# Kernel optimization log

Measured on AMD Instinct MI355X. Metric: run time of the kernel, lower is better.

The kernel has to match this reference:

```python
import jax, jax.numpy as jnp
import numpy as np
import math

B, N, D, H = 32, 512, 512, 8  # batch, num_neurons(=seq len=input_size), d_model, n_head
DH = D // H


def setup_inputs() -> dict:
    key = jax.random.key(0)
    ks = jax.random.split(key, 20)
    g = lambda k, shape, fan_in: jax.random.normal(k, shape, dtype=jnp.float32) / np.sqrt(fan_in)
    return {
        "x": jax.random.normal(ks[0], (B, N), dtype=jnp.float32),
        # per-neuron Linear(1, d_model): weight [N, D], bias [N, D]
        "W_emb": g(ks[1], (N, D), 1),
        "b_emb": g(ks[2], (N, D), 1),
        # MHA projections (stored [in, out])
        "Wq": g(ks[3], (D, D), D), "bq": jnp.zeros((D,), jnp.float32),
        "Wk": g(ks[4], (D, D), D), "bk": jnp.zeros((D,), jnp.float32),
        "Wv": g(ks[5], (D, D), D), "bv": jnp.zeros((D,), jnp.float32),
        "Wo": g(ks[6], (D, D), D), "bo": jnp.zeros((D,), jnp.float32),
        # per-neuron Linear(d_model, 1): weight [N, D], bias [N]
        "W_un": g(ks[7], (N, D), D),
        "b_un": jnp.zeros((N,), jnp.float32),
        # ff1: 512 -> 2048 -> 512 -> 256 (no activations)
        "W1": g(ks[8], (N, 2048), N), "b1": jnp.zeros((2048,), jnp.float32),
        "W2": g(ks[9], (2048, 512), 2048), "b2": jnp.zeros((512,), jnp.float32),
        "W3": g(ks[10], (512, 256), 512), "b3": jnp.zeros((256,), jnp.float32),
    }


def _forward(x, W_emb, b_emb, Wq, bq, Wk, bk, Wv, bv, Wo, bo, W_un, b_un, W1, b1, W2, b2, W3, b3):
    # Embedding: batched rank-1 'linear' per neuron -> [B, N, D]
    h = x[:, :, None] * W_emb[None] + b_emb[None]
    # MHA (note: positional encoding in the original is computed but unused)
    q = (h @ Wq + bq).reshape(B, N, H, DH).transpose(0, 2, 1, 3)
    k = (h @ Wk + bk).reshape(B, N, H, DH).transpose(0, 2, 1, 3)
    v = (h @ Wv + bv).reshape(B, N, H, DH).transpose(0, 2, 1, 3)
    scores = jnp.einsum('bhnd,bhmd->bhnm', q, k) / math.sqrt(DH)
    attn = jax.nn.softmax(scores, axis=-1)
    o = jnp.einsum('bhnm,bhmd->bhnd', attn, v)
    o = o.transpose(0, 2, 1, 3).reshape(B, N, D)
    o = o @ Wo + bo  # [B, N, D]
    # unEmbedding: per-neuron Linear(D, 1) -> [B, N, 1]
    x_atten = (jnp.einsum('bnd,nd->bn', o, W_un) + b_un)[:, :, None]
    # ff1 on squeezed [B, N]
    y = x_atten[..., 0]
    y = ((y @ W1 + b1) @ W2 + b2) @ W3 + b3  # [B, 256]
    y = y.reshape(-1, 1, 8, 32)
    # bilinear upsample to (16, 64), half-pixel centers (torch align_corners=False)
    y = jax.image.resize(y, (y.shape[0], 1, 16, 64), method='bilinear')
    y_min = y.min(axis=(2, 3), keepdims=True)
    y_max = y.max(axis=(2, 3), keepdims=True)
    y = (y - y_min) / (y_max - y_min + 1e-8)
    return y, x_atten


def reference(x, W_emb, b_emb, Wq, bq, Wk, bk, Wv, bv, Wo, bo, W_un, b_un, W1, b1, W2, b2, W3, b3):
    y, x_atten = _forward(x, W_emb, b_emb, Wq, bq, Wk, bk, Wv, bv, Wo, bo, W_un, b_un, W1, b1, W2, b2, W3, b3)
    # return_attn=False path: attention_weights is None (omitted)
    return (y, x_atten)
```

## Files before the change

### kernel.cpp

```cpp
#include <hip/hip_runtime.h>

#define B_  32
#define N_  512
#define D_  512
#define H_  8
#define DH_ 64
#define M_  (B_*N_)

typedef __attribute__((ext_vector_type(4))) float          f32x4;
typedef __attribute__((ext_vector_type(4))) unsigned short us4;
typedef __attribute__((ext_vector_type(8))) unsigned short us8;
typedef __attribute__((ext_vector_type(8))) __bf16         bf16x8;

__device__ __forceinline__ f32x4 mfma_bf16(us8 a, us8 b, f32x4 c) {
  return __builtin_amdgcn_mfma_f32_16x16x32_bf16(
      __builtin_bit_cast(bf16x8, a), __builtin_bit_cast(bf16x8, b), c, 0, 0, 0);
}

__device__ __forceinline__ unsigned short f2bf(float f) {
  return __builtin_bit_cast(unsigned short, (__bf16)f);
}

__device__ __forceinline__ float bf2f(unsigned short u) {
  return __builtin_bit_cast(float, (unsigned)u << 16);
}

__device__ __forceinline__ float fexp2(float x) {
  float r;
  asm("v_exp_f32 %0, %1" : "=v"(r) : "v"(x));
  return r;
}

__device__ __forceinline__ us8 ldg8(const unsigned short* p) {
  return *reinterpret_cast<const us8*>(p);
}

typedef const unsigned int __attribute__((address_space(1)))* gas_ptr;
typedef unsigned int __attribute__((address_space(3)))* las_ptr;

__device__ __forceinline__ void gload16(const unsigned short* src, unsigned short* ldsdst) {
  __builtin_amdgcn_global_load_lds((gas_ptr)(const void*)src, (las_ptr)(void*)ldsdst, 16, 0, 0);
}

__global__ __launch_bounds__(256) void k_pre(
    const float* __restrict__ W_emb, const float* __restrict__ b_emb,
    const float* __restrict__ Wun, const float* __restrict__ Wo,
    const float* __restrict__ Wq, const float* __restrict__ Wk,
    const float* __restrict__ Wv,
    const float* __restrict__ W1, const float* __restrict__ W2,
    const float* __restrict__ W3,
    const float* __restrict__ bo, const float* __restrict__ bun,
    unsigned short* __restrict__ P0, unsigned short* __restrict__ WunBf,
    unsigned short* __restrict__ WoBf, unsigned short* __restrict__ wT,
    unsigned short* __restrict__ w1T, unsigned short* __restrict__ w2T,
    unsigned short* __restrict__ w3T, float* __restrict__ cb,
    float* __restrict__ xa) {
  __shared__ float t[32][33];
  int id = blockIdx.x, tid = threadIdx.x;

  if (id < 1024) {
    int idx = id * 256 + tid;
    const float* src; unsigned short* dst; int off;
    if (idx < 65536)        { src = W_emb; dst = P0;          off = idx; }
    else if (idx < 131072)  { src = b_emb; dst = P0 + 262144; off = idx - 65536; }
    else if (idx < 196608)  { src = Wun;   dst = WunBf;       off = idx - 131072; }
    else                    { src = Wo;    dst = WoBf;        off = idx - 196608; }
    f32x4 v = *reinterpret_cast<const f32x4*>(src + (size_t)off * 4);
    us4 o;
#pragma unroll
    for (int e = 0; e < 4; ++e) o[e] = f2bf(v[e]);
    *reinterpret_cast<us4*>(dst + (size_t)off * 4) = o;
    return;
  }

  if (id >= 4096) {
    int idx = (id - 4096) * 256 + tid;
    *reinterpret_cast<f32x4*>(xa + (size_t)idx * 4) = (f32x4){0.f, 0.f, 0.f, 0.f};
    return;
  }

  if (id >= 3968) {
    int n = (id - 3968) * 4 + (tid >> 6);
    int lane = tid & 63;
    const float* a = Wun + (size_t)n * 512 + lane * 8;
    const float* b = bo + lane * 8;
    f32x4 a0 = *reinterpret_cast<const f32x4*>(a);
    f32x4 a1 = *reinterpret_cast<const f32x4*>(a + 4);
    f32x4 b0 = *reinterpret_cast<const f32x4*>(b);
    f32x4 b1 = *reinterpret_cast<const f32x4*>(b + 4);
    float s = a0[0]*b0[0] + a0[1]*b0[1] + a0[2]*b0[2] + a0[3]*b0[3]
            + a1[0]*b1[0] + a1[1]*b1[1] + a1[2]*b1[2] + a1[3]*b1[3];
#pragma unroll
    for (int off = 32; off; off >>= 1) s += __shfl_xor(s, off, 64);
    if (lane == 0) cb[n] = s + bun[n];
    return;
  }

  const float* src; unsigned short* dst; int R, C, bx, by;
  if (id < 1792) {
    int t3 = id - 1024, z = t3 >> 8, rem = t3 & 255;
    src = (z == 0) ? Wq : (z == 1) ? Wk : Wv;
    dst = wT + (size_t)z * (512 * 512);
    R = 512; C = 512; bx = rem & 15; by = rem >> 4;
  } else if (id < 2816) {
    int tr = id - 1792;
    src = W1; dst = w1T; R = 512; C = 2048; bx = tr & 63; by = tr >> 6;
  } else if (id < 3840) {
    int tr = id - 2816;
    src = W2; dst = w2T; R = 2048; C = 512; bx = tr & 15; by = tr >> 4;
  } else {
    int tr = id - 3840;
    src = W3; dst = w3T; R = 512; C = 256; bx = tr & 7; by = tr >> 3;
  }
  int c0 = bx * 32, r0 = by * 32;
  int tx = tid & 31, ty = tid >> 5;
  for (int yy = ty; yy < 32; yy += 8)
    t[yy][tx] = src[(size_t)(r0 + yy) * C + c0 + tx];
  __syncthreads();
  for (int yy = ty; yy < 32; yy += 8)
    dst[(size_t)(c0 + yy) * R + r0 + tx] = f2bf(t[tx][yy]);
}

__global__ __launch_bounds__(256, 4) void k_prep(
    const unsigned short* __restrict__ P0,
    const unsigned short* __restrict__ wT,
    const unsigned short* __restrict__ WunBf,
    const unsigned short* __restrict__ WoBf,
    const float* __restrict__ bq, const float* __restrict__ bk,
    const float* __restrict__ bv,
    unsigned short* __restrict__ P1,
    unsigned short* __restrict__ vpre,
    unsigned short* __restrict__ wEff) {
  __shared__ __align__(16) unsigned short lds[2][2 * 64 * 64];
  const int K = 512;
  int nwg = gridDim.x;
  int cpx = nwg >> 3;
  int wgid = ((int)blockIdx.x & 7) * cpx + ((int)blockIdx.x >> 3);
  bool p1 = wgid < 384;
  int lid = p1 ? wgid : wgid - 384;
  int ntiles = p1 ? 24 : 8;
  const unsigned short* A  = p1 ? P0 : WunBf;
  const unsigned short* Bt = p1 ? wT : WoBf;
  int mt = lid / ntiles, nt = lid - mt * ntiles;
  int m0 = mt * 64, n0 = nt * 64;
  int tid = threadIdx.x, wave = tid >> 6, lane = tid & 63;
  int lrow = lane & 15, g = lane >> 4;

  f32x4 acc[4];
#pragma unroll
  for (int i = 0; i < 4; ++i) acc[i] = (f32x4){0.f, 0.f, 0.f, 0.f};

  int rseg_base = wave * 8 + (lane >> 3);
  int coff = (((lane & 7) ^ (lane >> 3)) << 3);

#pragma unroll
  for (int i = 0; i < 2; ++i) {
    int rs = i * 32 + rseg_base;
    gload16(A  + (size_t)(m0 + rs) * K + coff, &lds[0][(i * 4 + wave) * 512]);
    gload16(Bt + (size_t)(n0 + rs) * K + coff, &lds[0][4096 + (i * 4 + wave) * 512]);
  }
  __syncthreads();

  for (int ks = 0; ks < 8; ++ks) {
    if (ks < 7) {
      int k0 = (ks + 1) * 64;
      int buf = (ks + 1) & 1;
#pragma unroll
      for (int i = 0; i < 2; ++i) {
        int rs = i * 32 + rseg_base;
        gload16(A  + (size_t)(m0 + rs) * K + k0 + coff, &lds[buf][(i * 4 + wave) * 512]);
        gload16(Bt + (size_t)(n0 + rs) * K + k0 + coff, &lds[buf][4096 + (i * 4 + wave) * 512]);
      }
    }
    const char* la = (const char*)&lds[ks & 1][0];
    const char* lb = la + 8192;
    int sw = (lrow & 7) << 4;
#pragma unroll
    for (int kk = 0; kk < 2; ++kk) {
      us8 aF = *reinterpret_cast<const us8*>(
          la + (wave * 16 + lrow) * 128 + ((kk * 64 + g * 16) ^ sw));
      us8 bF[4];
#pragma unroll
      for (int ni = 0; ni < 4; ++ni)
        bF[ni] = *reinterpret_cast<const us8*>(
            lb + (ni * 16 + lrow) * 128 + ((kk * 64 + g * 16) ^ sw));
#pragma unroll
      for (int ni = 0; ni < 4; ++ni)
        acc[ni] = mfma_bf16(aF, bF[ni], acc[ni]);
    }
    __syncthreads();
  }

  if (p1) {
#pragma unroll
    for (int ni = 0; ni < 4; ++ni) {
      int j = n0 + ni * 16 + lrow;
      int which = j >> 9, jj = j & 511;
      float bj = (which == 0 ? bq : which == 1 ? bk : bv)[jj];
#pragma unroll
      for (int r = 0; r < 4; ++r) {
        int mrow = m0 + wave * 16 + g * 4 + r;
        int isB = mrow >> 9, n = mrow & 511;
        unsigned short v16 = f2bf(acc[ni][r] + (isB ? bj : 0.f));
        if (which < 2) P1[(size_t)mrow * 1536 + j] = v16;
        else           vpre[(size_t)isB * 262144 + (size_t)jj * 512 + n] = v16;
      }
    }
  } else {
#pragma unroll
    for (int ni = 0; ni < 4; ++ni) {
      int j = n0 + ni * 16 + lrow;
#pragma unroll
      for (int r = 0; r < 4; ++r) {
        int mrow = m0 + wave * 16 + g * 4 + r;
        wEff[(size_t)mrow * 512 + j] = f2bf(acc[ni][r]);
      }
    }
  }
}

__global__ __launch_bounds__(256, 4) void k_attn(
    const float* __restrict__ x,
    const unsigned short* __restrict__ P1,
    const unsigned short* __restrict__ vpre,
    const unsigned short* __restrict__ wEff,
    float* __restrict__ xa) {
  __shared__ __align__(16) unsigned short kbuf[4096];
  __shared__ __align__(16) unsigned short vbuf[4096];
  __shared__ __align__(16) unsigned short pbuf[4][1024];
  int L = blockIdx.x;
  int bh = ((L & 7) << 5) | (L >> 5);
  int chunk = (L >> 3) & 3;
  int b = bh >> 3, h = bh & 7;
  int w = threadIdx.x >> 6, lane = threadIdx.x & 63;
  int lr = lane & 15, g = lane >> 4;
  const float cexp = 0.18033688011112042f;
  const float THRraw = 44.35f;
  const float* xb = x + b * 512;

  us8 bq[2][2];
#pragma unroll
  for (int tt = 0; tt < 2; ++tt) {
    int n = chunk * 128 + w * 32 + tt * 16 + lr;
    float xv = xb[n];
#pragma unroll
    for (int hh = 0; hh < 2; ++hh) {
      int col = h * 64 + hh * 32 + g * 8;
      us8 a = ldg8(P1 + (size_t)n * 1536 + col);
      us8 bb = ldg8(P1 + (size_t)(512 + n) * 1536 + col);
      us8 o8;
#pragma unroll
      for (int e = 0; e < 8; ++e) o8[e] = f2bf(xv * bf2f(a[e]) + bf2f(bb[e]));
      bq[tt][hh] = o8;
    }
  }

  f32x4 oacc[2][4];
#pragma unroll
  for (int tt = 0; tt < 2; ++tt)
#pragma unroll
    for (int db = 0; db < 4; ++db) oacc[tt][db] = (f32x4){0.f, 0.f, 0.f, 0.f};
  float mrun[2] = {-3.0e38f, -3.0e38f};
  float lrun[2] = {0.f, 0.f};

  int dhV = w * 16 + lr;
  const unsigned short* vp0 = vpre + (size_t)(h * 64 + dhV) * 512;
  const unsigned short* vp1 = vp0 + 262144;
  char* pw = (char*)&pbuf[w][0];

  for (int mb = 0; mb < 8; ++mb) {
    if (mb > 0) __syncthreads();

    int nK = mb * 64 + w * 16 + lr;
    float xk = xb[nK];
#pragma unroll
    for (int kk = 0; kk < 2; ++kk) {
      int col = 512 + h * 64 + kk * 32 + g * 8;
      us8 a = ldg8(P1 + (size_t)nK * 1536 + col);
      us8 bb = ldg8(P1 + (size_t)(512 + nK) * 1536 + col);
      us8 o8;
#pragma unroll
      for (int e = 0; e < 8; ++e) o8[e] = f2bf(xk * bf2f(a[e]) + bf2f(bb[e]));
      *reinterpret_cast<us8*>((char*)kbuf + (2 * w + kk) * 1024 + lane * 16) = o8;
    }
#pragma unroll
    for (int kk = 0; kk < 2; ++kk) {
      int n0 = mb * 64 + kk * 32 + g * 8;
      us8 a = ldg8(vp0 + n0);
      us8 bb = ldg8(vp1 + n0);
      f32x4 x0 = *reinterpret_cast<const f32x4*>(xb + n0);
      f32x4 x1 = *reinterpret_cast<const f32x4*>(xb + n0 + 4);
      us8 o8;
#pragma unroll
      for (int e = 0; e < 8; ++e) {
        float xe = (e < 4) ? x0[e] : x1[e - 4];
        o8[e] = f2bf(xe * bf2f(a[e]) + bf2f(bb[e]));
      }
      *reinterpret_cast<us8*>((char*)vbuf + (2 * w + kk) * 1024 + lane * 16) = o8;
    }
    __syncthreads();

    const char* kb = (const char*)kbuf;
    const char* vb = (const char*)vbuf;

#pragma unroll
    for (int tt = 0; tt < 2; ++tt) {
      f32x4 s[4];
      __builtin_amdgcn_s_setprio(1);
#pragma unroll
      for (int mc_l = 0; mc_l < 4; ++mc_l) {
        f32x4 a = (f32x4){0.f, 0.f, 0.f, 0.f};
        a = mfma_bf16(*(const us8*)(kb + (mc_l * 2 + 0) * 1024 + lane * 16), bq[tt][0], a);
        a = mfma_bf16(*(const us8*)(kb + (mc_l * 2 + 1) * 1024 + lane * 16), bq[tt][1], a);
        s[mc_l] = a;
      }
      __builtin_amdgcn_s_setprio(0);
      float pmax = fmaxf(fmaxf(s[0][0], s[0][1]), fmaxf(s[0][2], s[0][3]));
#pragma unroll
      for (int mc_l = 1; mc_l < 4; ++mc_l)
        pmax = fmaxf(pmax, fmaxf(fmaxf(s[mc_l][0], s[mc_l][1]), fmaxf(s[mc_l][2], s[mc_l][3])));
      pmax = fmaxf(pmax, __shfl_xor(pmax, 16, 64));
      pmax = fmaxf(pmax, __shfl_xor(pmax, 32, 64));
      if (__any(pmax > mrun[tt] + THRraw)) {
        float mnew = fmaxf(mrun[tt], pmax);
        float rs = fexp2((mrun[tt] - mnew) * cexp);
        mrun[tt] = mnew;
        lrun[tt] *= rs;
#pragma unroll
        for (int db = 0; db < 4; ++db) oacc[tt][db] *= rs;
      }
      float mcur = mrun[tt];
      float lsum = 0.f;
#pragma unroll
      for (int mc_l = 0; mc_l < 4; ++mc_l) {
#pragma unroll
        for (int r = 0; r < 4; ++r) {
          float p = fexp2((s[mc_l][r] - mcur) * cexp);
          s[mc_l][r] = p;
          lsum += p;
        }
      }
      lsum += __shfl_xor(lsum, 16, 64);
      lsum += __shfl_xor(lsum, 32, 64);
      lrun[tt] += lsum;
#pragma unroll
      for (int mc_l = 0; mc_l < 4; ++mc_l) {
        uint2 u;
        u.x = (unsigned)f2bf(s[mc_l][0]) | ((unsigned)f2bf(s[mc_l][1]) << 16);
        u.y = (unsigned)f2bf(s[mc_l][2]) | ((unsigned)f2bf(s[mc_l][3]) << 16);
        unsigned off = (unsigned)((mc_l >> 1) * 1024 + (((mc_l & 1) << 1) | (g >> 1)) * 256
                                  + lr * 16 + (g & 1) * 8);
        *reinterpret_cast<uint2*>(pw + off) = u;
      }
      __builtin_amdgcn_s_setprio(1);
#pragma unroll
      for (int ks = 0; ks < 2; ++ks) {
        us8 bp = *(const us8*)(pw + ks * 1024 + lane * 16);
#pragma unroll
        for (int db = 0; db < 4; ++db) {
          us8 av = *(const us8*)(vb + (db * 2 + ks) * 1024 + lane * 16);
          oacc[tt][db] = mfma_bf16(av, bp, oacc[tt][db]);
        }
      }
      __builtin_amdgcn_s_setprio(0);
    }
  }

#pragma unroll
  for (int tt = 0; tt < 2; ++tt) {
    float inv = 1.f / lrun[tt];
    int nmod = chunk * 128 + w * 32 + tt * 16 + lr;
    const unsigned short* wrow = wEff + (size_t)nmod * 512 + h * 64 + g * 4;
    float part = 0.f;
#pragma unroll
    for (int db = 0; db < 4; ++db) {
      us4 wv = *reinterpret_cast<const us4*>(wrow + db * 16);
#pragma unroll
      for (int r = 0; r < 4; ++r) part += oacc[tt][db][r] * bf2f(wv[r]);
    }
    part *= inv;
    part += __shfl_xor(part, 16, 64);
    part += __shfl_xor(part, 32, 64);
    if (g == 0) atomicAdd(&xa[b * 512 + nmod], part);
  }
}

__global__ __launch_bounds__(256) void k_xafin(
    const float* __restrict__ xa, const float* __restrict__ cb,
    float* __restrict__ out_xa, unsigned short* __restrict__ xabf) {
  int m = blockIdx.x * 256 + threadIdx.x;
  float v = xa[m] + cb[m & (N_ - 1)];
  out_xa[m] = v;
  xabf[m] = f2bf(v);
}

__global__ __launch_bounds__(256) void k_ffmm(
    const unsigned short* __restrict__ A,
    const unsigned short* __restrict__ Bt,
    const float* __restrict__ bias, int K, int N,
    unsigned short* __restrict__ obf) {
  int wave = threadIdx.x >> 6, lane = threadIdx.x & 63;
  int lrow = lane & 15, g = lane >> 4;
  int j = blockIdx.x * 64 + wave * 16 + lrow;
  f32x4 acc0 = (f32x4){0.f, 0.f, 0.f, 0.f}, acc1 = acc0;
  const unsigned short* brow = Bt + (size_t)j * K;
  for (int k0 = g * 8; k0 < K; k0 += 32) {
    us8 bfr = ldg8(brow + k0);
    acc0 = mfma_bf16(ldg8(A + (size_t)lrow * K + k0), bfr, acc0);
    acc1 = mfma_bf16(ldg8(A + (size_t)(16 + lrow) * K + k0), bfr, acc1);
  }
  float bj = bias[j];
#pragma unroll
  for (int r = 0; r < 4; ++r) {
    int mA = g * 4 + r, mB = 16 + g * 4 + r;
    obf[(size_t)mA * N + j] = f2bf(acc0[r] + bj);
    obf[(size_t)mB * N + j] = f2bf(acc1[r] + bj);
  }
}

__global__ __launch_bounds__(256) void k_ffmm2(
    const unsigned short* __restrict__ A,
    const unsigned short* __restrict__ Bt,
    float* __restrict__ y2p) {
  int ks = blockIdx.x >> 3, nb = blockIdx.x & 7;
  int wave = threadIdx.x >> 6, lane = threadIdx.x & 63;
  int lrow = lane & 15, g = lane >> 4;
  int j = nb * 64 + wave * 16 + lrow;
  const int K = 2048;
  f32x4 acc0 = (f32x4){0.f, 0.f, 0.f, 0.f}, acc1 = acc0;
  const unsigned short* brow = Bt + (size_t)j * K;
#pragma unroll
  for (int i = 0; i < 8; ++i) {
    int k0 = ks * 256 + i * 32 + g * 8;
    us8 bfr = ldg8(brow + k0);
    acc0 = mfma_bf16(ldg8(A + (size_t)lrow * K + k0), bfr, acc0);
    acc1 = mfma_bf16(ldg8(A + (size_t)(16 + lrow) * K + k0), bfr, acc1);
  }
  float* out = y2p + (size_t)ks * 16384;
#pragma unroll
  for (int r = 0; r < 4; ++r) {
    out[(size_t)(g * 4 + r) * 512 + j] = acc0[r];
    out[(size_t)(16 + g * 4 + r) * 512 + j] = acc1[r];
  }
}

__global__ __launch_bounds__(256) void k_ff3up(
    const float* __restrict__ y2p,
    const unsigned short* __restrict__ w3T,
    const float* __restrict__ b2, const float* __restrict__ b3,
    float* __restrict__ out) {
  __shared__ float y2l[512];
  __shared__ float y3[256];
  __shared__ float red[8];
  int b = blockIdx.x, t = threadIdx.x;
#pragma unroll
  for (int hh = 0; hh < 2; ++hh) {
    int d = t + hh * 256;
    float v = b2[d];
#pragma unroll
    for (int s = 0; s < 8; ++s) v += y2p[(size_t)s * 16384 + (size_t)b * 512 + d];
    y2l[d] = v;
  }
  __syncthreads();
  const unsigned short* wrow = w3T + (size_t)t * 512;
  float s = b3[t];
  for (int d8 = 0; d8 < 64; ++d8) {
    us8 wv = ldg8(wrow + d8 * 8);
#pragma unroll
    for (int e = 0; e < 8; ++e) s += y2l[d8 * 8 + e] * bf2f(wv[e]);
  }
  y3[t] = s;
  __syncthreads();
  float vals[4];
  float mn = 3.0e38f, mx = -3.0e38f;
#pragma unroll
  for (int p2 = 0; p2 < 4; ++p2) {
    int p = t * 4 + p2;
    int i = p >> 6, jj = p & 63;
    float sy = fmaxf((float)i * 0.5f - 0.25f, 0.0f);
    int y0 = (int)sy; float fy = sy - (float)y0;
    int y1i = min(y0 + 1, 7);
    float sx = fmaxf((float)jj * 0.5f - 0.25f, 0.0f);
    int x0 = (int)sx; float fx = sx - (float)x0;
    int x1 = min(x0 + 1, 31);
    float v00 = y3[y0 * 32 + x0], v01 = y3[y0 * 32 + x1];
    float v10 = y3[y1i * 32 + x0], v11 = y3[y1i * 32 + x1];
    float v = (1.f - fy) * ((1.f - fx) * v00 + fx * v01)
            +        fy  * ((1.f - fx) * v10 + fx * v11);
    vals[p2] = v;
    mn = fminf(mn, v); mx = fmaxf(mx, v);
  }
#pragma unroll
  for (int off = 32; off; off >>= 1) {
    mn = fminf(mn, __shfl_xor(mn, off, 64));
    mx = fmaxf(mx, __shfl_xor(mx, off, 64));
  }
  int wv2 = t >> 6;
  if ((t & 63) == 0) { red[wv2] = mn; red[4 + wv2] = mx; }
  __syncthreads();
  mn = fminf(fminf(red[0], red[1]), fminf(red[2], red[3]));
  mx = fmaxf(fmaxf(red[4], red[5]), fmaxf(red[6], red[7]));
  float inv = 1.f / (mx - mn + 1e-8f);
#pragma unroll
  for (int p2 = 0; p2 < 4; ++p2)
    out[(size_t)b * 1024 + t * 4 + p2] = (vals[p2] - mn) * inv;
}

extern "C" void kernel_launch(void* const* d_in, const int* in_sizes, int n_in,
                              void* d_out, int out_size, void* d_ws, size_t ws_size,
                              hipStream_t stream) {
  const float* x     = (const float*)d_in[0];
  const float* W_emb = (const float*)d_in[1];
  const float* b_emb = (const float*)d_in[2];
  const float* Wq    = (const float*)d_in[3];
  const float* bq    = (const float*)d_in[4];
  const float* Wk    = (const float*)d_in[5];
  const float* bk    = (const float*)d_in[6];
  const float* Wv    = (const float*)d_in[7];
  const float* bv    = (const float*)d_in[8];
  const float* Wo    = (const float*)d_in[9];
  const float* bo    = (const float*)d_in[10];
  const float* W_un  = (const float*)d_in[11];
  const float* b_un  = (const float*)d_in[12];
  const float* W1    = (const float*)d_in[13];
  const float* b1    = (const float*)d_in[14];
  const float* W2    = (const float*)d_in[15];
  const float* b2    = (const float*)d_in[16];
  const float* W3    = (const float*)d_in[17];
  const float* b3    = (const float*)d_in[18];

  char* ws = (char*)d_ws;
  unsigned short* P0    = (unsigned short*)(ws + 0);
  unsigned short* P1    = (unsigned short*)(ws + 1048576);
  unsigned short* vpre  = (unsigned short*)(ws + 4194304);
  unsigned short* WunBf = (unsigned short*)(ws + 5242880);
  unsigned short* WoBf  = (unsigned short*)(ws + 5767168);
  unsigned short* wT    = (unsigned short*)(ws + 67108864);
  unsigned short* wEff  = (unsigned short*)(ws + 68681728);
  float*          cb    = (float*)(ws + 69206016);
  unsigned short* xabf  = (unsigned short*)(ws + 69208064);
  float*          xa    = (float*)(ws + 69240832);
  unsigned short* w1T   = (unsigned short*)(ws + 83886080);
  unsigned short* w2T   = (unsigned short*)(ws + 85983232);
  unsigned short* w3T   = (unsigned short*)(ws + 88080384);
  unsigned short* y1bf  = (unsigned short*)(ws + 88342528);
  float*          y2p   = (float*)(ws + 94371840);

  float* out_y  = (float*)d_out;
  float* out_xa = ((float*)d_out) + 32768;

  k_pre<<<dim3(4112), dim3(256), 0, stream>>>(
      W_emb, b_emb, W_un, Wo, Wq, Wk, Wv, W1, W2, W3, bo, b_un,
      P0, WunBf, WoBf, wT, w1T, w2T, w3T, cb, xa);

  k_prep<<<dim3(448), dim3(256), 0, stream>>>(
      P0, wT, WunBf, WoBf, bq, bk, bv, P1, vpre, wEff);

  k_attn<<<dim3(1024), dim3(256), 0, stream>>>(x, P1, vpre, wEff, xa);

  k_xafin<<<dim3(64), dim3(256), 0, stream>>>(xa, cb, out_xa, xabf);

  k_ffmm<<<dim3(32), dim3(256), 0, stream>>>(xabf, w1T, b1, 512, 2048, y1bf);
  k_ffmm2<<<dim3(64), dim3(256), 0, stream>>>(y1bf, w2T, y2p);

  k_ff3up<<<dim3(B_), dim3(256), 0, stream>>>(y2p, w3T, b2, b3, out_y);
}
```

Before: 95.43 us.

## Double-buffer K/V tiles in attention kernel with register prefetch

Splits the K/V LDS staging into two buffers. Global loads for the next key block are issued into registers before the current block's MFMA work, and written into the alternate buffer after compute. The aim is to hide global-load latency behind the QK/PV math and drop one barrier per iteration. The cost is doubled LDS for K/V and more live registers, which may reduce occupancy under launch_bounds(256,4).

```diff
diff --git a/kernel.cpp b/kernel.cpp
--- a/kernel.cpp
+++ b/kernel.cpp
@@ -225,8 +225,8 @@
     const unsigned short* __restrict__ vpre,
     const unsigned short* __restrict__ wEff,
     float* __restrict__ xa) {
-  __shared__ __align__(16) unsigned short kbuf[4096];
-  __shared__ __align__(16) unsigned short vbuf[4096];
+  __shared__ __align__(16) unsigned short kbuf[2][4096];
+  __shared__ __align__(16) unsigned short vbuf[2][4096];
   __shared__ __align__(16) unsigned short pbuf[4][1024];
   int L = blockIdx.x;
   int bh = ((L & 7) << 5) | (L >> 5);
@@ -268,40 +268,64 @@
   const unsigned short* vp1 = vp0 + 262144;
   char* pw = (char*)&pbuf[w][0];
 
+  us8 pkA0, pkA1, pkB0, pkB1, pvA0, pvA1, pvB0, pvB1;
+  float pxk;
+  f32x4 pvx00, pvx01, pvx10, pvx11;
+
+#define ISSUE(mb_)                                                             \
+  {                                                                            \
+    int nK = (mb_) * 64 + w * 16 + lr;                                         \
+    pxk = xb[nK];                                                              \
+    int colb = 512 + h * 64 + g * 8;                                           \
+    pkA0 = ldg8(P1 + (size_t)nK * 1536 + colb);                                \
+    pkB0 = ldg8(P1 + (size_t)(512 + nK) * 1536 + colb);                        \
+    pkA1 = ldg8(P1 + (size_t)nK * 1536 + colb + 32);                           \
+    pkB1 = ldg8(P1 + (size_t)(512 + nK) * 1536 + colb + 32);                   \
+    int n0a = (mb_) * 64 + g * 8;                                              \
+    pvA0 = ldg8(vp0 + n0a);  pvB0 = ldg8(vp1 + n0a);                           \
+    pvx00 = *reinterpret_cast<const f32x4*>(xb + n0a);                         \
+    pvx01 = *reinterpret_cast<const f32x4*>(xb + n0a + 4);                     \
+    pvA1 = ldg8(vp0 + n0a + 32);  pvB1 = ldg8(vp1 + n0a + 32);                 \
+    pvx10 = *reinterpret_cast<const f32x4*>(xb + n0a + 32);                    \
+    pvx11 = *reinterpret_cast<const f32x4*>(xb + n0a + 36);                    \
+  }
+
+#define WRITEBUF(buf_)                                                         \
+  {                                                                            \
+    us8 o8;                                                                    \
+    _Pragma("unroll")                                                          \
+    for (int e = 0; e < 8; ++e) o8[e] = f2bf(pxk * bf2f(pkA0[e]) + bf2f(pkB0[e])); \
+    *reinterpret_cast<us8*>((char*)&kbuf[buf_][0] + (2 * w + 0) * 1024 + lane * 16) = o8; \
+    _Pragma("unroll")                                                          \
+    for (int e = 0; e < 8; ++e) o8[e] = f2bf(pxk * bf2f(pkA1[e]) + bf2f(pkB1[e])); \
+    *reinterpret_cast<us8*>((char*)&kbuf[buf_][0] + (2 * w + 1) * 1024 + lane * 16) = o8; \
+    _Pragma("unroll")                                                          \
+    for (int e = 0; e < 8; ++e) {                                              \
+      float xe = (e < 4) ? pvx00[e] : pvx01[e - 4];                            \
+      o8[e] = f2bf(xe * bf2f(pvA0[e]) + bf2f(pvB0[e]));                        \
+    }                                                                          \
+    *reinterpret_cast<us8*>((char*)&vbuf[buf_][0] + (2 * w + 0) * 1024 + lane * 16) = o8; \
+    _Pragma("unroll")                                                          \
+    for (int e = 0; e < 8; ++e) {                                              \
+      float xe = (e < 4) ? pvx10[e] : pvx11[e - 4];                            \
+      o8[e] = f2bf(xe * bf2f(pvA1[e]) + bf2f(pvB1[e]));                        \
+    }                                                                          \
+    *reinterpret_cast<us8*>((char*)&vbuf[buf_][0] + (2 * w + 1) * 1024 + lane * 16) = o8; \
+  }
+
+  ISSUE(0);
+  WRITEBUF(0);
+
   for (int mb = 0; mb < 8; ++mb) {
-    if (mb > 0) __syncthreads();
-
-    int nK = mb * 64 + w * 16 + lr;
-    float xk = xb[nK];
-#pragma unroll
-    for (int kk = 0; kk < 2; ++kk) {
-      int col = 512 + h * 64 + kk * 32 + g * 8;
-      us8 a = ldg8(P1 + (size_t)nK * 1536 + col);
-      us8 bb = ldg8(P1 + (size_t)(512 + nK) * 1536 + col);
-      us8 o8;
-#pragma unroll
-      for (int e = 0; e < 8; ++e) o8[e] = f2bf(xk * bf2f(a[e]) + bf2f(bb[e]));
-      *reinterpret_cast<us8*>((char*)kbuf + (2 * w + kk) * 1024 + lane * 16) = o8;
-    }
-#pragma unroll
-    for (int kk = 0; kk < 2; ++kk) {
-      int n0 = mb * 64 + kk * 32 + g * 8;
-      us8 a = ldg8(vp0 + n0);
-      us8 bb = ldg8(vp1 + n0);
-      f32x4 x0 = *reinterpret_cast<const f32x4*>(xb + n0);
-      f32x4 x1 = *reinterpret_cast<const f32x4*>(xb + n0 + 4);
-      us8 o8;
-#pragma unroll
-      for (int e = 0; e < 8; ++e) {
-        float xe = (e < 4) ? x0[e] : x1[e - 4];
-        o8[e] = f2bf(xe * bf2f(a[e]) + bf2f(bb[e]));
-      }
-      *reinterpret_cast<us8*>((char*)vbuf + (2 * w + kk) * 1024 + lane * 16) = o8;
+    int cur = mb & 1;
+    if (mb < 7) {
+      ISSUE(mb + 1);
+      __builtin_amdgcn_sched_barrier(0);
     }
     __syncthreads();
 
-    const char* kb = (const char*)kbuf;
-    const char* vb = (const char*)vbuf;
+    const char* kb = (const char*)&kbuf[cur][0];
+    const char* vb = (const char*)&vbuf[cur][0];
 
 #pragma unroll
     for (int tt = 0; tt < 2; ++tt) {
@@ -364,6 +388,10 @@
       }
       __builtin_amdgcn_s_setprio(0);
     }
+
+    if (mb < 7) {
+      WRITEBUF(cur ^ 1);
+    }
   }
 
 #pragma unroll
@@ -383,6 +411,8 @@
     part += __shfl_xor(part, 32, 64);
     if (g == 0) atomicAdd(&xa[b * 512 + nmod], part);
   }
+#undef ISSUE
+#undef WRITEBUF
 }
 
 __global__ __launch_bounds__(256) void k_xafin(
```

New measurement: 119.4 us. 1.25x slower.
